# Optimization experiments

Measured on AMD Instinct MI355X. Metric: run time of the kernel, lower is better.

The kernel has to match this reference:

```python
import jax, jax.numpy as jnp
import numpy as np

B, N, T = 512, 128, 64
ALPHA = 0.5  # LeakyReLU negative slope
NEG = jnp.float32(-9e15)


def _gat(h, mask, W, a):
    # GraphAttentionLayer with concat=True (trailing relu), eval mode (no dropout)
    Wh = h @ W                                   # [B,N,F]
    F = W.shape[1]
    e1 = Wh @ a[:F]                              # [B,N,1]
    e2 = Wh @ a[F:]                              # [B,N,1]
    e = jax.nn.leaky_relu(e1 + jnp.swapaxes(e2, 1, 2), ALPHA)  # [B,N,N]
    e = jnp.where(mask, e, NEG)
    att = jax.nn.softmax(e, axis=1)              # torch softmax dim=1 (over rows)
    return jax.nn.relu(jnp.matmul(att, Wh))


def _lstm_layer(x, wih, whh, bih, bhh):
    # x: [T,B,in]; hidden size 1; torch gate order i,f,g,o
    h0 = jnp.zeros((x.shape[1], 1), x.dtype)
    def step(carry, xt):
        h, c = carry
        g = xt @ wih.T + h @ whh.T + bih + bhh   # [B,4]
        i, f, gg, o = jnp.split(g, 4, axis=-1)
        c = jax.nn.sigmoid(f) * c + jax.nn.sigmoid(i) * jnp.tanh(gg)
        h = jax.nn.sigmoid(o) * jnp.tanh(c)
        return (h, c), h
    _, ys = jax.lax.scan(step, (h0, h0), x)
    return ys                                    # [T,B,1]


def setup_inputs() -> dict:
    key = jax.random.key(0)
    ks = jax.random.split(key, 32)
    def xu(k, shape, gain=1.414):
        lim = gain * np.sqrt(6.0 / (shape[0] + shape[1]))
        return jax.random.uniform(k, shape, jnp.float32, -lim, lim)
    d = {}
    d["adjacency"] = jax.random.randint(ks[0], (B, N, N), 0, 2, dtype=jnp.int32)
    d["feature"] = jax.random.normal(ks[1], (B, N), jnp.float32)
    d["time"] = jax.random.normal(ks[2], (B, N), jnp.float32)
    d["interval_popularity"] = jax.random.normal(ks[3], (B, T), jnp.float32)
    # GAT params
    d["W1"] = xu(ks[4], (1, 512)); d["a1"] = xu(ks[5], (1024, 1))
    d["W2"] = xu(ks[6], (512, 8)); d["a2"] = xu(ks[7], (16, 1))
    # attention-pooling params (torch.randn in original)
    d["Weight"] = jax.random.normal(ks[8], (128, 128), jnp.float32)
    d["Wv"] = jax.random.normal(ks[9], (128, 128), jnp.float32)
    # 2-layer LSTM(1->1)
    d["wih0"] = jax.random.normal(ks[10], (4, 1)) * 0.5
    d["whh0"] = jax.random.normal(ks[11], (4, 1)) * 0.5
    d["bih0"] = jax.random.normal(ks[12], (4,)) * 0.5
    d["bhh0"] = jax.random.normal(ks[13], (4,)) * 0.5
    d["wih1"] = jax.random.normal(ks[14], (4, 1)) * 0.5
    d["whh1"] = jax.random.normal(ks[15], (4, 1)) * 0.5
    d["bih1"] = jax.random.normal(ks[16], (4,)) * 0.5
    d["bhh1"] = jax.random.normal(ks[17], (4,)) * 0.5
    # MultiheadAttention(embed_dim=1, heads=1)
    d["mha_in_w"] = jax.random.normal(ks[18], (3, 1)) * 0.5
    d["mha_in_b"] = jnp.zeros((3,), jnp.float32)
    d["mha_out_w"] = jax.random.normal(ks[19], (1, 1)) * 0.5
    d["mha_out_b"] = jnp.zeros((1,), jnp.float32)
    # FL MLP: 192->128->32->1 (stored as [in,out])
    d["fl1_w"] = xu(ks[20], (192, 128), 1.0); d["fl1_b"] = jnp.zeros((128,), jnp.float32)
    d["fl2_w"] = xu(ks[21], (128, 32), 1.0);  d["fl2_b"] = jnp.zeros((32,), jnp.float32)
    d["fl3_w"] = xu(ks[22], (32, 1), 1.0);    d["fl3_b"] = jnp.zeros((1,), jnp.float32)
    return d


def reference(adjacency, feature, time, interval_popularity,
              W1, a1, W2, a2, Weight, Wv,
              wih0, whh0, bih0, bhh0, wih1, whh1, bih1, bhh1,
              mha_in_w, mha_in_b, mha_out_w, mha_out_b,
              fl1_w, fl1_b, fl2_w, fl2_b, fl3_w, fl3_b):
    mask = adjacency > 0
    x = feature.reshape(B, N, -1)                # [B,128,1]
    h = _gat(x, mask, W1, a1)                    # [B,128,512]
    h = jax.nn.relu(h)
    h = _gat(h, mask, W2, a2)                    # [B,128,8]

    xs = jnp.swapaxes(interval_popularity.reshape(B, -1, 1), 0, 1)  # [T,B,1]
    xs = _lstm_layer(xs, wih0, whh0, bih0, bhh0)
    xs = _lstm_layer(xs, wih1, whh1, bih1, bhh1)
    ip = jnp.swapaxes(xs, 0, 1).reshape(B, -1)   # [B,64]

    h = jnp.mean(h, axis=2, keepdims=True)       # [B,128,1]
    Wt = time.reshape(B, N, -1)                  # [B,128,1]
    att = jnp.concatenate([h, Wt], axis=2)       # [B,128,2]
    att = jnp.swapaxes(jnp.swapaxes(att, 1, 2) @ Weight, 1, 2)  # [B,128,2]
    att = jax.nn.softmax(att, axis=2)
    hv = jnp.swapaxes(jnp.concatenate([h, Wt], axis=2), 1, 2)   # [B,2,128]
    hv = jax.nn.relu((hv @ Wv).reshape(B, N, -1))  # faithful reshape (not transpose)
    h = jnp.sum(hv * att, axis=2)                # [B,128]

    h = jnp.concatenate([h, ip], axis=1)         # [B,192]
    hq = h[..., None]                            # [B,192,1]
    q = hq * mha_in_w[0, 0] + mha_in_b[0]
    k = hq * mha_in_w[1, 0] + mha_in_b[1]
    v = hq * mha_in_w[2, 0] + mha_in_b[2]
    a = jax.nn.softmax(q @ jnp.swapaxes(k, 1, 2), axis=-1)  # scale=1/sqrt(1)
    ho = (a @ v) * mha_out_w[0, 0] + mha_out_b[0]
    h = (ho + hq).reshape(B, -1)                 # [B,192]

    h = jax.nn.relu(h @ fl1_w + fl1_b)
    h = jnp.tanh(h @ fl2_w + fl2_b)
    h = jax.nn.relu(h @ fl3_w + fl3_b)           # [B,1]
    return h
```

## Files before the change

kernel.cpp:

```cpp
#include <hip/hip_runtime.h>
#include <math.h>

typedef unsigned int uint;
typedef unsigned long long ull;

#define L2E 1.44269504f

__device__ __forceinline__ float lrelu(float z){ return fmaxf(z, 0.5f*z); }
__device__ __forceinline__ float reluf(float z){ return fmaxf(z, 0.f); }
__device__ __forceinline__ float fexp(float z){ return __builtin_amdgcn_exp2f(z*L2E); }
__device__ __forceinline__ float frcp(float z){ return __builtin_amdgcn_rcpf(z); }
__device__ __forceinline__ float tanh_n(float z){
  return __fmaf_rn(2.f, __builtin_amdgcn_rcpf(1.f + __builtin_amdgcn_exp2f(-2.f*L2E*z)), -1.f);
}

__global__ __launch_bounds__(256) void fused_kernel(
    const int* __restrict__ adj, const float* __restrict__ feat,
    const float* __restrict__ timei,
    const float* __restrict__ Weight, const float* __restrict__ Wv,
    const float* __restrict__ W1, const float* __restrict__ a1,
    const float* __restrict__ W2, const float* __restrict__ a2,
    const float* __restrict__ ipop,
    const float* __restrict__ wih0, const float* __restrict__ whh0,
    const float* __restrict__ bih0, const float* __restrict__ bhh0,
    const float* __restrict__ wih1, const float* __restrict__ whh1,
    const float* __restrict__ bih1, const float* __restrict__ bhh1,
    const float* __restrict__ mha_in_w, const float* __restrict__ mha_in_b,
    const float* __restrict__ mha_out_w, const float* __restrict__ mha_out_b,
    const float* __restrict__ fl1_w, const float* __restrict__ fl1_b,
    const float* __restrict__ fl2_w, const float* __restrict__ fl2_b,
    const float* __restrict__ fl3_w, const float* __restrict__ fl3_b,
    float* __restrict__ out)
{
  const int b = blockIdx.x, t = threadIdx.x;
  const int lane = t & 127, h = t >> 7;
  const int wv = t >> 6, ln = t & 63;

  __shared__ ull   rowW[256];
  __shared__ float xs[128], tim[128], hm[128], eAs[128], thr1[128];
  __shared__ float2 f2a[128];
  __shared__ float2 red2[2][128];
  __shared__ float4 q4[128];
  __shared__ float4 pool4[2][128];
  __shared__ float2 kv[192];
  __shared__ float  hq[192], h2s[192];
  __shared__ float  sred[8];
  __shared__ float  cpart[4][2];
  __shared__ float  pqpart[4][16];
  __shared__ float  cons[24];
  __shared__ float  ips[64];

  if (t < 128){ xs[t] = feat[b*128 + t]; tim[t] = timei[b*128 + t]; }

  float a2reg[16];
  if (t == 0){
    #pragma unroll
    for (int g = 0; g < 16; ++g) a2reg[g] = a2[g];
  }

  float h1v=0.f, c1s=0.f, h2v=0.f, c2s=0.f;
  float wi0s[4], wh0s[4], bb0s[4], wi1s[4], wh1s[4], bb1s[4];
  const float4* xsrc4 = (const float4*)(ipop + b*64);
  float4 xcur0, xcur1;
  if (t == 255){
    #pragma unroll
    for (int k = 0; k < 4; ++k){
      const float s = (k == 2) ? -2.f*L2E : -L2E;
      wi0s[k]=wih0[k]*s; wh0s[k]=whh0[k]*s; bb0s[k]=(bih0[k]+bhh0[k])*s;
      wi1s[k]=wih1[k]*s; wh1s[k]=whh1[k]*s; bb1s[k]=(bih1[k]+bhh1[k])*s;
    }
    xcur0 = xsrc4[0]; xcur1 = xsrc4[1];
  }
  auto lstm8 = [&](int c){
    if (t != 255) return;
    const float4 xa = xcur0, xb = xcur1;
    if (c < 7){ xcur0 = xsrc4[2*c+2]; xcur1 = xsrc4[2*c+3]; }
    float o[8];
    #pragma unroll
    for (int si = 0; si < 8; ++si){
      const float x = (si==0)?xa.x:(si==1)?xa.y:(si==2)?xa.z:(si==3)?xa.w:
                      (si==4)?xb.x:(si==5)?xb.y:(si==6)?xb.z:xb.w;
      float gi = frcp(1.f + __builtin_amdgcn_exp2f(__fmaf_rn(x, wi0s[0], __fmaf_rn(h1v, wh0s[0], bb0s[0]))));
      float gf = frcp(1.f + __builtin_amdgcn_exp2f(__fmaf_rn(x, wi0s[1], __fmaf_rn(h1v, wh0s[1], bb0s[1]))));
      float gg = __fmaf_rn(2.f, frcp(1.f + __builtin_amdgcn_exp2f(__fmaf_rn(x, wi0s[2], __fmaf_rn(h1v, wh0s[2], bb0s[2])))), -1.f);
      float go = frcp(1.f + __builtin_amdgcn_exp2f(__fmaf_rn(x, wi0s[3], __fmaf_rn(h1v, wh0s[3], bb0s[3]))));
      c1s = gf*c1s + gi*gg;  h1v = go*tanh_n(c1s);
      float hi = frcp(1.f + __builtin_amdgcn_exp2f(__fmaf_rn(h1v, wi1s[0], __fmaf_rn(h2v, wh1s[0], bb1s[0]))));
      float hf = frcp(1.f + __builtin_amdgcn_exp2f(__fmaf_rn(h1v, wi1s[1], __fmaf_rn(h2v, wh1s[1], bb1s[1]))));
      float hg = __fmaf_rn(2.f, frcp(1.f + __builtin_amdgcn_exp2f(__fmaf_rn(h1v, wi1s[2], __fmaf_rn(h2v, wh1s[2], bb1s[2])))), -1.f);
      float ho = frcp(1.f + __builtin_amdgcn_exp2f(__fmaf_rn(h1v, wi1s[3], __fmaf_rn(h2v, wh1s[3], bb1s[3]))));
      c2s = hf*c2s + hi*hg;  h2v = ho*tanh_n(c2s);
      o[si] = h2v;
    }
    #pragma unroll
    for (int si = 0; si < 8; ++si) ips[8*c + si] = o[si];
  };

  {
    const int* abase = adj + (((long)b) << 14) + wv*4096 + ln;
    ull myword = 0;
    #pragma unroll
    for (int blk = 0; blk < 8; ++blk){
      int v[8];
      #pragma unroll
      for (int q = 0; q < 8; ++q) v[q] = abase[(blk*8 + q)*64];
      #pragma unroll
      for (int q = 0; q < 8; ++q){
        ull m = __ballot(v[q] > 0);
        myword = (ln == blk*8 + q) ? m : myword;
      }
    }
    rowW[t] = myword;
  }

  {
    float w0 = W1[t], w1 = W1[t+256];
    float s1 = __fmaf_rn(w0, a1[t],     w1*a1[t+256]);
    float s2 = __fmaf_rn(w0, a1[512+t], w1*a1[768+t]);
    #pragma unroll
    for (int off = 32; off; off >>= 1){ s1 += __shfl_xor(s1, off); s2 += __shfl_xor(s2, off); }
    if (ln == 0){ cpart[wv][0] = s1; cpart[wv][1] = s2; }
  }
  {
    float accP[8], accQ[8];
    #pragma unroll
    for (int g = 0; g < 8; ++g){ accP[g] = 0.f; accQ[g] = 0.f; }
    #pragma unroll
    for (int e = 0; e < 2; ++e){
      const int f = 2*t + e;
      const float w = W1[f];
      const float wp = fmaxf(w, 0.f), wn = fminf(w, 0.f);
      const float4 A = *(const float4*)(W2 + f*8);
      const float4 Bv = *(const float4*)(W2 + f*8 + 4);
      accP[0]=__fmaf_rn(wp,A.x,accP[0]);  accQ[0]=__fmaf_rn(wn,A.x,accQ[0]);
      accP[1]=__fmaf_rn(wp,A.y,accP[1]);  accQ[1]=__fmaf_rn(wn,A.y,accQ[1]);
      accP[2]=__fmaf_rn(wp,A.z,accP[2]);  accQ[2]=__fmaf_rn(wn,A.z,accQ[2]);
      accP[3]=__fmaf_rn(wp,A.w,accP[3]);  accQ[3]=__fmaf_rn(wn,A.w,accQ[3]);
      accP[4]=__fmaf_rn(wp,Bv.x,accP[4]); accQ[4]=__fmaf_rn(wn,Bv.x,accQ[4]);
      accP[5]=__fmaf_rn(wp,Bv.y,accP[5]); accQ[5]=__fmaf_rn(wn,Bv.y,accQ[5]);
      accP[6]=__fmaf_rn(wp,Bv.z,accP[6]); accQ[6]=__fmaf_rn(wn,Bv.z,accQ[6]);
      accP[7]=__fmaf_rn(wp,Bv.w,accP[7]); accQ[7]=__fmaf_rn(wn,Bv.w,accQ[7]);
    }
    #pragma unroll
    for (int g = 0; g < 8; ++g){
      float p = accP[g], q = accQ[g];
      #pragma unroll
      for (int off = 32; off; off >>= 1){ p += __shfl_xor(p, off); q += __shfl_xor(q, off); }
      if (ln == 0){ pqpart[wv][g] = p; pqpart[wv][8+g] = q; }
    }
  }
  __syncthreads();

  const ull rowm = rowW[lane*2 + h];
  ull colm = 0;
  {
    const int wsel = lane >> 6, bsel = lane & 63;
    #pragma unroll 8
    for (int k = 0; k < 64; ++k)
      colm |= ((rowW[(64*h + k)*2 + wsel] >> bsel) & 1ull) << k;
  }
  if (t < 64){
    float mx = fmaxf(xs[t], xs[t+64]);
    float mn = fminf(xs[t], xs[t+64]);
    #pragma unroll
    for (int off = 32; off; off >>= 1){
      mx = fmaxf(mx, __shfl_xor(mx, off));
      mn = fminf(mn, __shfl_xor(mn, off));
    }
    if (t == 0){ sred[0] = mx; sred[1] = mn; }
  }
  if (t == 0){
    float c1v = cpart[0][0]+cpart[1][0]+cpart[2][0]+cpart[3][0];
    float c2v = cpart[0][1]+cpart[1][1]+cpart[2][1]+cpart[3][1];
    cons[0] = c1v; cons[1] = c2v;
    float pAx=0.f, qAx=0.f, pBx=0.f, qBx=0.f;
    #pragma unroll
    for (int g = 0; g < 8; ++g){
      float P = pqpart[0][g]+pqpart[1][g]+pqpart[2][g]+pqpart[3][g];
      float Q = pqpart[0][8+g]+pqpart[1][8+g]+pqpart[2][8+g]+pqpart[3][8+g];
      cons[2+g] = P; cons[10+g] = Q;
      pAx = __fmaf_rn(P, a2reg[g],   pAx);  qAx = __fmaf_rn(Q, a2reg[g],   qAx);
      pBx = __fmaf_rn(P, a2reg[8+g], pBx);  qBx = __fmaf_rn(Q, a2reg[8+g], qBx);
    }
    cons[18]=pAx; cons[19]=qAx; cons[20]=pBx; cons[21]=qBx;
  }
  lstm8(0);
  __syncthreads();

  float myE1=0.f, myEh=0.f, myA=0.f, myB=0.f, mythr=0.f, myx=0.f;
  {
    const float c1 = cons[0], c2 = cons[1];
    const float rmax = (c1 >= 0.f) ? c1*sred[0] : c1*sred[1];
    if (t < 128){
      myx = xs[t];
      float r  = c1*myx;
      float cj = c2*myx;
      float cb = lrelu(rmax + cj);
      myE1  = fexp(r - rmax);
      myEh  = fexp(0.5f*(r - rmax));
      myA   = fexp(rmax + cj - cb);
      myB   = fexp(0.5f*(rmax + cj) - cb);
      mythr = fexp(-cj - rmax);
      f2a[t] = make_float2(myE1, myEh);
      thr1[t] = mythr;
    }
  }
  lstm8(1);
  __syncthreads();

  {
    const float thrj = thr1[lane];
    float s1 = 0.f, s2 = 0.f;
    #pragma unroll 8
    for (int k = 0; k < 64; ++k){
      float2 E = f2a[64*h + k];
      bool m = ((colm >> k) & 1ull);
      bool cond = (E.x >= thrj);
      s1 += (m &&  cond) ? E.x : 0.f;
      s2 += (m && !cond) ? E.y : 0.f;
    }
    red2[h][lane] = make_float2(s1, s2);
  }
  lstm8(2);
  __syncthreads();

  if (t < 128){
    float2 a = red2[0][t], bb = red2[1][t];
    float den = __fmaf_rn(myA, a.x + bb.x, myB*(a.y + bb.y));
    float cr = frcp(den);
    q4[t] = make_float4(myA*cr*myx, myB*cr*myx, mythr, 0.f);
  }
  lstm8(3);
  __syncthreads();

  {
    const float2 Eo = f2a[lane];
    float t1 = 0.f, t2 = 0.f;
    #pragma unroll 8
    for (int k = 0; k < 64; ++k){
      float4 G = q4[64*h + k];
      bool m = ((rowm >> k) & 1ull);
      bool cond = (Eo.x >= G.z);
      t1 += (m &&  cond) ? G.x : 0.f;
      t2 += (m && !cond) ? G.y : 0.f;
    }
    red2[h][lane] = make_float2(t1, t2);
  }
  lstm8(4);
  __syncthreads();

  float u = 0.f, eBv = 0.f, eAv = 0.f;
  if (t < 128){
    float2 a = red2[0][t], bb = red2[1][t];
    u = __fmaf_rn(myE1, a.x + bb.x, myEh*(a.y + bb.y));
    eAv = (u >= 0.f ? cons[18] : cons[19])*u;
    eBv = (u >= 0.f ? cons[20] : cons[21])*u;
    eAs[t] = eAv;
  }
  lstm8(5);
  __syncthreads();

  if (t < 64){
    float mx = fmaxf(eAs[t], eAs[t+64]);
    #pragma unroll
    for (int off = 32; off; off >>= 1) mx = fmaxf(mx, __shfl_xor(mx, off));
    if (t == 0) sred[2] = mx;
  }
  lstm8(6);
  __syncthreads();

  float myE1b=0.f, myEhb=0.f, myA2=0.f, myB2=0.f;
  {
    const float eAmax = sred[2];
    if (t < 128){
      float cb = lrelu(eAmax + eBv);
      myE1b = fexp(eAv - eAmax);
      myEhb = fexp(0.5f*(eAv - eAmax));
      myA2  = fexp(eAmax + eBv - cb);
      myB2  = fexp(0.5f*(eAmax + eBv) - cb);
      float th = fexp(-eBv - eAmax);
      f2a[t] = make_float2(myE1b, myEhb);
      thr1[t] = th;
    }
  }
  lstm8(7);
  __syncthreads();

  {
    const float thrj = thr1[lane];
    float s1 = 0.f, s2 = 0.f;
    #pragma unroll 8
    for (int k = 0; k < 64; ++k){
      float2 E = f2a[64*h + k];
      bool m = ((colm >> k) & 1ull);
      bool cond = (E.x >= thrj);
      s1 += (m &&  cond) ? E.x : 0.f;
      s2 += (m && !cond) ? E.y : 0.f;
    }
    red2[h][lane] = make_float2(s1, s2);
  }
  __syncthreads();

  if (t < 128){
    float2 a = red2[0][t], bb = red2[1][t];
    float den = __fmaf_rn(myA2, a.x + bb.x, myB2*(a.y + bb.y));
    float cr = frcp(den);
    float up = fmaxf(u, 0.f), un = fminf(u, 0.f);
    q4[t] = make_float4(myA2*cr*up, myB2*cr*up, myA2*cr*un, myB2*cr*un);
  }
  __syncthreads();

  {
    const float2 Eo = f2a[lane];
    float sp1=0.f, sp2=0.f, sn1=0.f, sn2=0.f;
    #pragma unroll 8
    for (int k = 0; k < 64; ++k){
      int j = 64*h + k;
      float4 G = q4[j];
      float thj = thr1[j];
      bool m = ((rowm >> k) & 1ull);
      bool cond = (Eo.x >= thj);
      sp1 += (m &&  cond) ? G.x : 0.f;
      sp2 += (m && !cond) ? G.y : 0.f;
      sn1 += (m &&  cond) ? G.z : 0.f;
      sn2 += (m && !cond) ? G.w : 0.f;
    }
    pool4[h][lane] = make_float4(sp1, sp2, sn1, sn2);
  }
  __syncthreads();

  if (t < 128){
    float4 a = pool4[0][t], bb = pool4[1][t];
    float sp = __fmaf_rn(myE1b, a.x + bb.x, myEhb*(a.y + bb.y));
    float sn = __fmaf_rn(myE1b, a.z + bb.z, myEhb*(a.w + bb.w));
    float acc = 0.f;
    #pragma unroll
    for (int g = 0; g < 8; ++g) acc += reluf(__fmaf_rn(sp, cons[2+g], sn*cons[10+g]));
    hm[t] = 0.125f*acc;
  }
  __syncthreads();

  {
    const int n = lane;
    float a0=0.f, a1v=0.f, v0=0.f, v1=0.f;
    const int m0 = h*64;
    #pragma unroll 4
    for (int k = 0; k < 64; ++k){
      int m = m0 + k;
      float hmv = hm[m], tv = tim[m];
      float wg = Weight[(m<<7) + n], wvv = Wv[(m<<7) + n];
      a0 = __fmaf_rn(hmv, wg, a0); a1v = __fmaf_rn(tv, wg, a1v);
      v0 = __fmaf_rn(hmv, wvv, v0); v1 = __fmaf_rn(tv, wvv, v1);
    }
    pool4[h][n] = make_float4(a0, a1v, v0, v1);
  }
  __syncthreads();

  float att0 = 0.f, att1 = 0.f, rsv = 0.f;
  if (t < 128){
    float4 a = pool4[0][t], bb = pool4[1][t];
    float A0 = a.x + bb.x, A1 = a.y + bb.y;
    red2[0][t] = make_float2(a.z + bb.z, a.w + bb.w);
    float mx = fmaxf(A0, A1);
    att0 = fexp(A0 - mx); att1 = fexp(A1 - mx);
    rsv = frcp(att0 + att1);
  }
  __syncthreads();

  if (t < 128){
    float r0, r1;
    if (t < 64){ r0 = red2[0][2*t].x;     r1 = red2[0][2*t+1].x; }
    else       { r0 = red2[0][2*t-128].y; r1 = red2[0][2*t-127].y; }
    hq[t] = (reluf(r0)*att0 + reluf(r1)*att1)*rsv;
  }
  if (t >= 192) hq[128 + (t - 192)] = ips[t - 192];
  __syncthreads();

  const float wq = mha_in_w[0], wk = mha_in_w[1], wvv_ = mha_in_w[2];
  const float bq = mha_in_b[0], bk = mha_in_b[1], bv = mha_in_b[2];
  const float wo = mha_out_w[0], bo = mha_out_b[0];
  if (t < 192){
    float hv_ = hq[t];
    kv[t] = make_float2(__fmaf_rn(hv_, wk, bk), __fmaf_rn(hv_, wvv_, bv));
  }
  __syncthreads();

  if (t < 64){
    float k0 = kv[t].x, k1 = kv[t+64].x, k2 = kv[t+128].x;
    float mx = fmaxf(fmaxf(k0, k1), k2);
    float mn = fminf(fminf(k0, k1), k2);
    #pragma unroll
    for (int off = 32; off; off >>= 1){
      mx = fmaxf(mx, __shfl_xor(mx, off));
      mn = fminf(mn, __shfl_xor(mn, off));
    }
    if (t == 0){ sred[3] = mx; sred[4] = mn; }
  }
  __syncthreads();

  if (t < 192){
    float hv_ = hq[t];
    float qi = __fmaf_rn(hv_, wq, bq);
    float mx = (qi >= 0.f) ? qi*sred[3] : qi*sred[4];
    const float qi2 = qi*L2E, mx2 = mx*L2E;
    float den = 0.f, num = 0.f;
    #pragma unroll 8
    for (int j = 0; j < 192; ++j){
      float2 K = kv[j];
      float e = __builtin_amdgcn_exp2f(__fmaf_rn(qi2, K.x, -mx2));
      den += e; num = __fmaf_rn(e, K.y, num);
    }
    h2s[t] = __fmaf_rn(num*frcp(den), wo, bo) + hv_;
  }
  __syncthreads();

  {
    const int n = t & 127;
    float acc = 0.f;
    const int i0 = h*96;
    #pragma unroll 8
    for (int k = 0; k < 96; ++k){
      int i = i0 + k;
      acc = __fmaf_rn(h2s[i], fl1_w[i*128 + n], acc);
    }
    red2[h][n].x = acc;
  }
  __syncthreads();

  if (t < 128) thr1[t] = reluf(red2[0][t].x + red2[1][t].x + fl1_b[t]);
  __syncthreads();

  if (t < 128){
    const int n = t & 31, seg = t >> 5;
    float p = 0.f;
    #pragma unroll 8
    for (int k = 0; k < 32; ++k){
      int i = seg*32 + k;
      p = __fmaf_rn(thr1[i], fl2_w[i*32 + n], p);
    }
    eAs[t] = p;
  }
  __syncthreads();

  if (t < 32) hm[t] = tanh_n(eAs[t] + eAs[t+32] + eAs[t+64] + eAs[t+96] + fl2_b[t]);
  __syncthreads();

  if (t < 64){
    float p = (t < 32) ? hm[t]*fl3_w[t] : 0.f;
    #pragma unroll
    for (int off = 32; off; off >>= 1) p += __shfl_xor(p, off);
    if (t == 0) out[b] = reluf(p + fl3_b[0]);
  }
}

extern "C" void kernel_launch(void* const* d_in, const int* in_sizes, int n_in,
                              void* d_out, int out_size, void* d_ws, size_t ws_size,
                              hipStream_t stream) {
  const int*   adj    = (const int*)  d_in[0];
  const float* feat   = (const float*)d_in[1];
  const float* timei  = (const float*)d_in[2];
  const float* ipop   = (const float*)d_in[3];
  const float* W1     = (const float*)d_in[4];
  const float* a1     = (const float*)d_in[5];
  const float* W2     = (const float*)d_in[6];
  const float* a2     = (const float*)d_in[7];
  const float* Weight = (const float*)d_in[8];
  const float* Wv     = (const float*)d_in[9];
  const float* wih0   = (const float*)d_in[10];
  const float* whh0   = (const float*)d_in[11];
  const float* bih0   = (const float*)d_in[12];
  const float* bhh0   = (const float*)d_in[13];
  const float* wih1   = (const float*)d_in[14];
  const float* whh1   = (const float*)d_in[15];
  const float* bih1   = (const float*)d_in[16];
  const float* bhh1   = (const float*)d_in[17];
  const float* mha_in_w  = (const float*)d_in[18];
  const float* mha_in_b  = (const float*)d_in[19];
  const float* mha_out_w = (const float*)d_in[20];
  const float* mha_out_b = (const float*)d_in[21];
  const float* fl1_w = (const float*)d_in[22];
  const float* fl1_b = (const float*)d_in[23];
  const float* fl2_w = (const float*)d_in[24];
  const float* fl2_b = (const float*)d_in[25];
  const float* fl3_w = (const float*)d_in[26];
  const float* fl3_b = (const float*)d_in[27];

  fused_kernel<<<512, 256, 0, stream>>>(adj, feat, timei, Weight, Wv,
                                        W1, a1, W2, a2, ipop,
                                        wih0, whh0, bih0, bhh0,
                                        wih1, whh1, bih1, bhh1,
                                        mha_in_w, mha_in_b, mha_out_w, mha_out_b,
                                        fl1_w, fl1_b, fl2_w, fl2_b, fl3_w, fl3_b,
                                        (float*)d_out);
}
```

Baseline: 49.36 us.

## Double block size to 512 threads and split inner loops four ways

Raises the per-graph block from 256 to 512 threads. The mask-build, attention, pooling, MHA and fl1 loops are split across 4 (or 2) partitions with shared-memory partial sums, and adjacency masks are kept as 32-bit chunks. The aim is to shorten the serial per-thread loop chains inside each block. In exchange it adds extra reductions and shared memory, and the LSTM thread still runs serially, which may bound the gain.

```diff
diff --git a/kernel.cpp b/kernel.cpp
--- a/kernel.cpp
+++ b/kernel.cpp
@@ -14,7 +14,7 @@
   return __fmaf_rn(2.f, __builtin_amdgcn_rcpf(1.f + __builtin_amdgcn_exp2f(-2.f*L2E*z)), -1.f);
 }
 
-__global__ __launch_bounds__(256) void fused_kernel(
+__global__ __launch_bounds__(512) void fused_kernel(
     const int* __restrict__ adj, const float* __restrict__ feat,
     const float* __restrict__ timei,
     const float* __restrict__ Weight, const float* __restrict__ Wv,
@@ -39,14 +39,15 @@
   __shared__ ull   rowW[256];
   __shared__ float xs[128], tim[128], hm[128], eAs[128], thr1[128];
   __shared__ float2 f2a[128];
-  __shared__ float2 red2[2][128];
+  __shared__ float2 red4[4][128];
   __shared__ float4 q4[128];
-  __shared__ float4 pool4[2][128];
+  __shared__ float4 pool4[4][128];
   __shared__ float2 kv[192];
   __shared__ float  hq[192], h2s[192];
+  __shared__ float  pden[2][192], pnum[2][192];
   __shared__ float  sred[8];
-  __shared__ float  cpart[4][2];
-  __shared__ float  pqpart[4][16];
+  __shared__ float  cpart[8][2];
+  __shared__ float  pqpart[8][16];
   __shared__ float  cons[24];
   __shared__ float  ips[64];
 
@@ -62,7 +63,7 @@
   float wi0s[4], wh0s[4], bb0s[4], wi1s[4], wh1s[4], bb1s[4];
   const float4* xsrc4 = (const float4*)(ipop + b*64);
   float4 xcur0, xcur1;
-  if (t == 255){
+  if (t == 511){
     #pragma unroll
     for (int k = 0; k < 4; ++k){
       const float s = (k == 2) ? -2.f*L2E : -L2E;
@@ -72,7 +73,7 @@
     xcur0 = xsrc4[0]; xcur1 = xsrc4[1];
   }
   auto lstm8 = [&](int c){
-    if (t != 255) return;
+    if (t != 511) return;
     const float4 xa = xcur0, xb = xcur1;
     if (c < 7){ xcur0 = xsrc4[2*c+2]; xcur1 = xsrc4[2*c+3]; }
     float o[8];
@@ -88,7 +89,7 @@
       float hi = frcp(1.f + __builtin_amdgcn_exp2f(__fmaf_rn(h1v, wi1s[0], __fmaf_rn(h2v, wh1s[0], bb1s[0]))));
       float hf = frcp(1.f + __builtin_amdgcn_exp2f(__fmaf_rn(h1v, wi1s[1], __fmaf_rn(h2v, wh1s[1], bb1s[1]))));
       float hg = __fmaf_rn(2.f, frcp(1.f + __builtin_amdgcn_exp2f(__fmaf_rn(h1v, wi1s[2], __fmaf_rn(h2v, wh1s[2], bb1s[2])))), -1.f);
-      float ho = frcp(1.f + __builtin_amdgcn_exp2f(__fmaf_rn(h1v, wi1s[3], __fmaf_rn(h2v, wh1s[3], bb1s[3]))));
+      float ho = frcp(1.f + __builtin_amdgcn_exp2f(__fmaf_rn(h1v, wi1s[3], __fmaf_rn(h2v, wh1s[3], bb1s[3])))) ;
       c2s = hf*c2s + hi*hg;  h2v = ho*tanh_n(c2s);
       o[si] = h2v;
     }
@@ -97,10 +98,10 @@
   };
 
   {
-    const int* abase = adj + (((long)b) << 14) + wv*4096 + ln;
+    const int* abase = adj + (((long)b) << 14) + wv*2048 + ln;
     ull myword = 0;
     #pragma unroll
-    for (int blk = 0; blk < 8; ++blk){
+    for (int blk = 0; blk < 4; ++blk){
       int v[8];
       #pragma unroll
       for (int q = 0; q < 8; ++q) v[q] = abase[(blk*8 + q)*64];
@@ -110,37 +111,27 @@
         myword = (ln == blk*8 + q) ? m : myword;
       }
     }
-    rowW[t] = myword;
-  }
-
-  {
-    float w0 = W1[t], w1 = W1[t+256];
-    float s1 = __fmaf_rn(w0, a1[t],     w1*a1[t+256]);
-    float s2 = __fmaf_rn(w0, a1[512+t], w1*a1[768+t]);
+    if (ln < 32) rowW[wv*32 + ln] = myword;
+  }
+
+  {
+    float w0 = W1[t];
+    float s1 = w0*a1[t];
+    float s2 = w0*a1[512+t];
     #pragma unroll
     for (int off = 32; off; off >>= 1){ s1 += __shfl_xor(s1, off); s2 += __shfl_xor(s2, off); }
     if (ln == 0){ cpart[wv][0] = s1; cpart[wv][1] = s2; }
   }
   {
+    const float w = W1[t];
+    const float wp = fmaxf(w, 0.f), wn = fminf(w, 0.f);
+    const float4 A = *(const float4*)(W2 + t*8);
+    const float4 Bv = *(const float4*)(W2 + t*8 + 4);
     float accP[8], accQ[8];
-    #pragma unroll
-    for (int g = 0; g < 8; ++g){ accP[g] = 0.f; accQ[g] = 0.f; }
-    #pragma unroll
-    for (int e = 0; e < 2; ++e){
-      const int f = 2*t + e;
-      const float w = W1[f];
-      const float wp = fmaxf(w, 0.f), wn = fminf(w, 0.f);
-      const float4 A = *(const float4*)(W2 + f*8);
-      const float4 Bv = *(const float4*)(W2 + f*8 + 4);
-      accP[0]=__fmaf_rn(wp,A.x,accP[0]);  accQ[0]=__fmaf_rn(wn,A.x,accQ[0]);
-      accP[1]=__fmaf_rn(wp,A.y,accP[1]);  accQ[1]=__fmaf_rn(wn,A.y,accQ[1]);
-      accP[2]=__fmaf_rn(wp,A.z,accP[2]);  accQ[2]=__fmaf_rn(wn,A.z,accQ[2]);
-      accP[3]=__fmaf_rn(wp,A.w,accP[3]);  accQ[3]=__fmaf_rn(wn,A.w,accQ[3]);
-      accP[4]=__fmaf_rn(wp,Bv.x,accP[4]); accQ[4]=__fmaf_rn(wn,Bv.x,accQ[4]);
-      accP[5]=__fmaf_rn(wp,Bv.y,accP[5]); accQ[5]=__fmaf_rn(wn,Bv.y,accQ[5]);
-      accP[6]=__fmaf_rn(wp,Bv.z,accP[6]); accQ[6]=__fmaf_rn(wn,Bv.z,accQ[6]);
-      accP[7]=__fmaf_rn(wp,Bv.w,accP[7]); accQ[7]=__fmaf_rn(wn,Bv.w,accQ[7]);
-    }
+    accP[0]=wp*A.x;  accQ[0]=wn*A.x;   accP[1]=wp*A.y;  accQ[1]=wn*A.y;
+    accP[2]=wp*A.z;  accQ[2]=wn*A.z;   accP[3]=wp*A.w;  accQ[3]=wn*A.w;
+    accP[4]=wp*Bv.x; accQ[4]=wn*Bv.x;  accP[5]=wp*Bv.y; accQ[5]=wn*Bv.y;
+    accP[6]=wp*Bv.z; accQ[6]=wn*Bv.z;  accP[7]=wp*Bv.w; accQ[7]=wn*Bv.w;
     #pragma unroll
     for (int g = 0; g < 8; ++g){
       float p = accP[g], q = accQ[g];
@@ -151,13 +142,13 @@
   }
   __syncthreads();
 
-  const ull rowm = rowW[lane*2 + h];
-  ull colm = 0;
+  const uint rowm = (uint)(rowW[lane*2 + (h>>1)] >> ((h&1)*32));
+  uint colm = 0;
   {
     const int wsel = lane >> 6, bsel = lane & 63;
     #pragma unroll 8
-    for (int k = 0; k < 64; ++k)
-      colm |= ((rowW[(64*h + k)*2 + wsel] >> bsel) & 1ull) << k;
+    for (int k = 0; k < 32; ++k)
+      colm |= (uint)((rowW[(32*h + k)*2 + wsel] >> bsel) & 1ull) << k;
   }
   if (t < 64){
     float mx = fmaxf(xs[t], xs[t+64]);
@@ -170,14 +161,16 @@
     if (t == 0){ sred[0] = mx; sred[1] = mn; }
   }
   if (t == 0){
-    float c1v = cpart[0][0]+cpart[1][0]+cpart[2][0]+cpart[3][0];
-    float c2v = cpart[0][1]+cpart[1][1]+cpart[2][1]+cpart[3][1];
+    float c1v = 0.f, c2v = 0.f;
+    #pragma unroll
+    for (int wvi = 0; wvi < 8; ++wvi){ c1v += cpart[wvi][0]; c2v += cpart[wvi][1]; }
     cons[0] = c1v; cons[1] = c2v;
     float pAx=0.f, qAx=0.f, pBx=0.f, qBx=0.f;
     #pragma unroll
     for (int g = 0; g < 8; ++g){
-      float P = pqpart[0][g]+pqpart[1][g]+pqpart[2][g]+pqpart[3][g];
-      float Q = pqpart[0][8+g]+pqpart[1][8+g]+pqpart[2][8+g]+pqpart[3][8+g];
+      float P = 0.f, Q = 0.f;
+      #pragma unroll
+      for (int wvi = 0; wvi < 8; ++wvi){ P += pqpart[wvi][g]; Q += pqpart[wvi][8+g]; }
       cons[2+g] = P; cons[10+g] = Q;
       pAx = __fmaf_rn(P, a2reg[g],   pAx);  qAx = __fmaf_rn(Q, a2reg[g],   qAx);
       pBx = __fmaf_rn(P, a2reg[8+g], pBx);  qBx = __fmaf_rn(Q, a2reg[8+g], qBx);
@@ -212,21 +205,23 @@
     const float thrj = thr1[lane];
     float s1 = 0.f, s2 = 0.f;
     #pragma unroll 8
-    for (int k = 0; k < 64; ++k){
-      float2 E = f2a[64*h + k];
-      bool m = ((colm >> k) & 1ull);
+    for (int k = 0; k < 32; ++k){
+      float2 E = f2a[32*h + k];
+      bool m = ((colm >> k) & 1u);
       bool cond = (E.x >= thrj);
       s1 += (m &&  cond) ? E.x : 0.f;
       s2 += (m && !cond) ? E.y : 0.f;
     }
-    red2[h][lane] = make_float2(s1, s2);
+    red4[h][lane] = make_float2(s1, s2);
   }
   lstm8(2);
   __syncthreads();
 
   if (t < 128){
-    float2 a = red2[0][t], bb = red2[1][t];
-    float den = __fmaf_rn(myA, a.x + bb.x, myB*(a.y + bb.y));
+    float sx = 0.f, sy = 0.f;
+    #pragma unroll
+    for (int g = 0; g < 4; ++g){ float2 v = red4[g][t]; sx += v.x; sy += v.y; }
+    float den = __fmaf_rn(myA, sx, myB*sy);
     float cr = frcp(den);
     q4[t] = make_float4(myA*cr*myx, myB*cr*myx, mythr, 0.f);
   }
@@ -237,22 +232,24 @@
     const float2 Eo = f2a[lane];
     float t1 = 0.f, t2 = 0.f;
     #pragma unroll 8
-    for (int k = 0; k < 64; ++k){
-      float4 G = q4[64*h + k];
-      bool m = ((rowm >> k) & 1ull);
+    for (int k = 0; k < 32; ++k){
+      float4 G = q4[32*h + k];
+      bool m = ((rowm >> k) & 1u);
       bool cond = (Eo.x >= G.z);
       t1 += (m &&  cond) ? G.x : 0.f;
       t2 += (m && !cond) ? G.y : 0.f;
     }
-    red2[h][lane] = make_float2(t1, t2);
+    red4[h][lane] = make_float2(t1, t2);
   }
   lstm8(4);
   __syncthreads();
 
   float u = 0.f, eBv = 0.f, eAv = 0.f;
   if (t < 128){
-    float2 a = red2[0][t], bb = red2[1][t];
-    u = __fmaf_rn(myE1, a.x + bb.x, myEh*(a.y + bb.y));
+    float sx = 0.f, sy = 0.f;
+    #pragma unroll
+    for (int g = 0; g < 4; ++g){ float2 v = red4[g][t]; sx += v.x; sy += v.y; }
+    u = __fmaf_rn(myE1, sx, myEh*sy);
     eAv = (u >= 0.f ? cons[18] : cons[19])*u;
     eBv = (u >= 0.f ? cons[20] : cons[21])*u;
     eAs[t] = eAv;
@@ -290,20 +287,22 @@
     const float thrj = thr1[lane];
     float s1 = 0.f, s2 = 0.f;
     #pragma unroll 8
-    for (int k = 0; k < 64; ++k){
-      float2 E = f2a[64*h + k];
-      bool m = ((colm >> k) & 1ull);
+    for (int k = 0; k < 32; ++k){
+      float2 E = f2a[32*h + k];
+      bool m = ((colm >> k) & 1u);
       bool cond = (E.x >= thrj);
       s1 += (m &&  cond) ? E.x : 0.f;
       s2 += (m && !cond) ? E.y : 0.f;
     }
-    red2[h][lane] = make_float2(s1, s2);
-  }
-  __syncthreads();
-
-  if (t < 128){
-    float2 a = red2[0][t], bb = red2[1][t];
-    float den = __fmaf_rn(myA2, a.x + bb.x, myB2*(a.y + bb.y));
+    red4[h][lane] = make_float2(s1, s2);
+  }
+  __syncthreads();
+
+  if (t < 128){
+    float sx = 0.f, sy = 0.f;
+    #pragma unroll
+    for (int g = 0; g < 4; ++g){ float2 v = red4[g][t]; sx += v.x; sy += v.y; }
+    float den = __fmaf_rn(myA2, sx, myB2*sy);
     float cr = frcp(den);
     float up = fmaxf(u, 0.f), un = fminf(u, 0.f);
     q4[t] = make_float4(myA2*cr*up, myB2*cr*up, myA2*cr*un, myB2*cr*un);
@@ -314,11 +313,11 @@
     const float2 Eo = f2a[lane];
     float sp1=0.f, sp2=0.f, sn1=0.f, sn2=0.f;
     #pragma unroll 8
-    for (int k = 0; k < 64; ++k){
-      int j = 64*h + k;
+    for (int k = 0; k < 32; ++k){
+      int j = 32*h + k;
       float4 G = q4[j];
       float thj = thr1[j];
-      bool m = ((rowm >> k) & 1ull);
+      bool m = ((rowm >> k) & 1u);
       bool cond = (Eo.x >= thj);
       sp1 += (m &&  cond) ? G.x : 0.f;
       sp2 += (m && !cond) ? G.y : 0.f;
@@ -330,9 +329,11 @@
   __syncthreads();
 
   if (t < 128){
-    float4 a = pool4[0][t], bb = pool4[1][t];
-    float sp = __fmaf_rn(myE1b, a.x + bb.x, myEhb*(a.y + bb.y));
-    float sn = __fmaf_rn(myE1b, a.z + bb.z, myEhb*(a.w + bb.w));
+    float sx=0.f, sy=0.f, sz=0.f, sw=0.f;
+    #pragma unroll
+    for (int g = 0; g < 4; ++g){ float4 v = pool4[g][t]; sx+=v.x; sy+=v.y; sz+=v.z; sw+=v.w; }
+    float sp = __fmaf_rn(myE1b, sx, myEhb*sy);
+    float sn = __fmaf_rn(myE1b, sz, myEhb*sw);
     float acc = 0.f;
     #pragma unroll
     for (int g = 0; g < 8; ++g) acc += reluf(__fmaf_rn(sp, cons[2+g], sn*cons[10+g]));
@@ -343,9 +344,9 @@
   {
     const int n = lane;
     float a0=0.f, a1v=0.f, v0=0.f, v1=0.f;
-    const int m0 = h*64;
+    const int m0 = h*32;
     #pragma unroll 4
-    for (int k = 0; k < 64; ++k){
+    for (int k = 0; k < 32; ++k){
       int m = m0 + k;
       float hmv = hm[m], tv = tim[m];
       float wg = Weight[(m<<7) + n], wvv = Wv[(m<<7) + n];
@@ -358,9 +359,10 @@
 
   float att0 = 0.f, att1 = 0.f, rsv = 0.f;
   if (t < 128){
-    float4 a = pool4[0][t], bb = pool4[1][t];
-    float A0 = a.x + bb.x, A1 = a.y + bb.y;
-    red2[0][t] = make_float2(a.z + bb.z, a.w + bb.w);
+    float A0=0.f, A1=0.f, V0=0.f, V1=0.f;
+    #pragma unroll
+    for (int g = 0; g < 4; ++g){ float4 v = pool4[g][t]; A0+=v.x; A1+=v.y; V0+=v.z; V1+=v.w; }
+    red4[0][t] = make_float2(V0, V1);
     float mx = fmaxf(A0, A1);
     att0 = fexp(A0 - mx); att1 = fexp(A1 - mx);
     rsv = frcp(att0 + att1);
@@ -369,11 +371,11 @@
 
   if (t < 128){
     float r0, r1;
-    if (t < 64){ r0 = red2[0][2*t].x;     r1 = red2[0][2*t+1].x; }
-    else       { r0 = red2[0][2*t-128].y; r1 = red2[0][2*t-127].y; }
+    if (t < 64){ r0 = red4[0][2*t].x;     r1 = red4[0][2*t+1].x; }
+    else       { r0 = red4[0][2*t-128].y; r1 = red4[0][2*t-127].y; }
     hq[t] = (reluf(r0)*att0 + reluf(r1)*att1)*rsv;
   }
-  if (t >= 192) hq[128 + (t - 192)] = ips[t - 192];
+  if (t >= 192 && t < 256) hq[128 + (t - 192)] = ips[t - 192];
   __syncthreads();
 
   const float wq = mha_in_w[0], wk = mha_in_w[1], wvv_ = mha_in_w[2];
@@ -398,36 +400,44 @@
   }
   __syncthreads();
 
-  if (t < 192){
-    float hv_ = hq[t];
-    float qi = __fmaf_rn(hv_, wq, bq);
+  if (t < 384){
+    const int half = (t >= 192), tt = t - half*192;
+    float qi = __fmaf_rn(hq[tt], wq, bq);
     float mx = (qi >= 0.f) ? qi*sred[3] : qi*sred[4];
     const float qi2 = qi*L2E, mx2 = mx*L2E;
     float den = 0.f, num = 0.f;
-    #pragma unroll 8
-    for (int j = 0; j < 192; ++j){
-      float2 K = kv[j];
+    const int j0 = half*96;
+    #pragma unroll 8
+    for (int jj = 0; jj < 96; ++jj){
+      float2 K = kv[j0 + jj];
       float e = __builtin_amdgcn_exp2f(__fmaf_rn(qi2, K.x, -mx2));
       den += e; num = __fmaf_rn(e, K.y, num);
     }
-    h2s[t] = __fmaf_rn(num*frcp(den), wo, bo) + hv_;
-  }
-  __syncthreads();
-
-  {
-    const int n = t & 127;
+    pden[half][tt] = den; pnum[half][tt] = num;
+  }
+  __syncthreads();
+
+  if (t < 192){
+    float den = pden[0][t] + pden[1][t];
+    float num = pnum[0][t] + pnum[1][t];
+    h2s[t] = __fmaf_rn(num*frcp(den), wo, bo) + hq[t];
+  }
+  __syncthreads();
+
+  {
+    const int n = t & 127, qtr = t >> 7;
     float acc = 0.f;
-    const int i0 = h*96;
-    #pragma unroll 8
-    for (int k = 0; k < 96; ++k){
+    const int i0 = qtr*48;
+    #pragma unroll 8
+    for (int k = 0; k < 48; ++k){
       int i = i0 + k;
       acc = __fmaf_rn(h2s[i], fl1_w[i*128 + n], acc);
     }
-    red2[h][n].x = acc;
-  }
-  __syncthreads();
-
-  if (t < 128) thr1[t] = reluf(red2[0][t].x + red2[1][t].x + fl1_b[t]);
+    red4[qtr][n].x = acc;
+  }
+  __syncthreads();
+
+  if (t < 128) thr1[t] = reluf(red4[0][t].x + red4[1][t].x + red4[2][t].x + red4[3][t].x + fl1_b[t]);
   __syncthreads();
 
   if (t < 128){
@@ -485,7 +495,7 @@
   const float* fl3_w = (const float*)d_in[26];
   const float* fl3_b = (const float*)d_in[27];
 
-  fused_kernel<<<512, 256, 0, stream>>>(adj, feat, timei, Weight, Wv,
+  fused_kernel<<<512, 512, 0, stream>>>(adj, feat, timei, Weight, Wv,
                                         W1, a1, W2, a2, ipop,
                                         wih0, whh0, bih0, bhh0,
                                         wih1, whh1, bih1, bhh1,
```

Result: faster. 43.90 us (-11.1%).
